# Performance work log

Measured on AMD Instinct MI355X. Metric: run time of the kernel, lower is better.

Reference implementation:

```python
import jax, jax.numpy as jnp
import numpy as np

DROPOUT_P = 0.1
DROPOUT_KEY = jax.random.key(42)


def setup_inputs() -> dict:
    key = jax.random.key(0)
    kq, kk, kv = jax.random.split(key, 3)
    B, S, H, D = 2, 2048, 16, 64
    query = jax.random.normal(kq, (B, S, H, D), dtype=jnp.float32)
    k_in = jax.random.normal(kk, (B, S, H, D), dtype=jnp.float32)
    value = jax.random.normal(kv, (B, S, H, D), dtype=jnp.float32)
    inv_scale_factor = jnp.asarray(8.0, dtype=jnp.float32)  # sqrt(head_dim)
    return {"query": query, "key": k_in, "value": value,
            "inv_scale_factor": inv_scale_factor}


def reference(query, key, value, inv_scale_factor):
    # permute(0,2,1,3): [B, S, H, D] -> [B, H, S, D]
    q = jnp.transpose(query, (0, 2, 1, 3))
    k = jnp.transpose(key, (0, 2, 1, 3))
    v = jnp.transpose(value, (0, 2, 1, 3))
    # scores: [B, H, S, S]
    scores = jnp.einsum("bhsd,bhtd->bhst", q, k) / inv_scale_factor
    attn = jax.nn.softmax(scores, axis=-1)
    # dropout (train mode, inverted scaling) with a fixed key
    keep = jax.random.bernoulli(DROPOUT_KEY, 1.0 - DROPOUT_P, attn.shape)
    attn = jnp.where(keep, attn / (1.0 - DROPOUT_P), 0.0)
    # output: [B, H, S, D]
    return jnp.einsum("bhst,bhtd->bhsd", attn, v)
```

## Files before the change

kernel.cpp:

```cpp
#include <hip/hip_runtime.h>
#include <hip/hip_bf16.h>
#include <stdint.h>

typedef __attribute__((ext_vector_type(8))) short short8;
typedef __attribute__((ext_vector_type(4))) float f32x4;
typedef __attribute__((ext_vector_type(4))) uint32_t u32x4;
typedef __attribute__((ext_vector_type(2))) uint32_t u32x2;

#define KEEP_TH 0xE6666600u

__device__ __forceinline__ uint32_t pkbf(float lo, float hi) {
  uint32_t r;
  asm("v_cvt_pk_bf16_f32 %0, %1, %2" : "=v"(r) : "v"(lo), "v"(hi));
  return r;
}

__device__ __forceinline__ uint32_t tf_bits(uint32_t x1pre) {
  uint32_t x1 = x1pre;
  uint32_t x0 = x1;
  x1 = __builtin_rotateleft32(x1, 13) ^ x0;
#define R(r) { x0 += x1; x1 = __builtin_rotateleft32(x1, (r)) ^ x0; }
  R(15) R(26) R(6)
  x0 += 42u;          x1 += 0x1BD11BF0u + 1u;
  R(17) R(29) R(16) R(24)
  x0 += 0x1BD11BF0u;  x1 += 2u;
  R(13) R(15) R(26) R(6)
                      x1 += 42u + 3u;
  R(17) R(29) R(16) R(24)
  x0 += 42u;          x1 += 0x1BD11BF0u + 4u;
  R(13) R(15) R(26) R(6)
  x0 += 0x1BD11BF0u;  x1 += 5u;
#undef R
  return x0 ^ x1;
}


__global__ __launch_bounds__(256, 4)
void attn_dropout_kernel(const float* __restrict__ Qg, const float* __restrict__ Kg,
                         const float* __restrict__ Vg, const float* __restrict__ invs,
                         float* __restrict__ Out) {
  __shared__ __align__(16) uint32_t KbF[512 * 4];
  __shared__ __align__(16) uint32_t VtF[512 * 4];
  __shared__ __align__(16) uint32_t PlF[512 * 4];

  const int tid = threadIdx.x;
  const int w = tid >> 6;
  const int l = tid & 63;
  const int e = l & 15;
  const int g = l >> 4;

  const int n  = blockIdx.x;
  const int bh = (n & 7) * 4 + ((n >> 3) & 3);
  const int b  = bh >> 4;
  const int h  = bh & 15;
  const int qc = n >> 5;
  const int qbase = qc * 64;

  const float c = 1.4426950408889634f / invs[0];
  const int sq = qbase + w * 16 + e;

  short8 qf[2];
#pragma unroll
  for (int kc = 0; kc < 2; ++kc) {
    const float* qp = Qg + (((b * 2048 + sq) * 16 + h) * 64 + kc * 32 + 8 * g);
    f32x4 q0 = *(const f32x4*)qp;
    f32x4 q1 = *(const f32x4*)(qp + 4);
    u32x4 u;
    u.x = pkbf(q0.x * c, q0.y * c);
    u.y = pkbf(q0.z * c, q0.w * c);
    u.z = pkbf(q1.x * c, q1.y * c);
    u.w = pkbf(q1.z * c, q1.w * c);
    qf[kc] = __builtin_bit_cast(short8, u);
  }

  f32x4 acc[4];
#pragma unroll
  for (int dt = 0; dt < 4; ++dt) acc[dt] = (f32x4){0.f, 0.f, 0.f, 0.f};
  float ls[4] = {0.f, 0.f, 0.f, 0.f};

  const uint32_t fb = ((uint32_t)b << 26) | ((uint32_t)h << 22) | ((uint32_t)sq << 11);

  const int s_e = tid & 15, s_g = (tid >> 4) & 3, s_kc = (tid >> 6) & 1, s_T = tid >> 7;
  const int v_e = tid & 15, v_gk = (tid >> 4) & 7, v_dt = tid >> 7;

  const float* kbase = Kg + (((b * 2048 + s_T * 16 + s_e) * 16 + h) * 64 + s_kc * 32 + 8 * s_g);
  const float* vbase = Vg + (((b * 2048 + 8 * v_gk) * 16 + h) * 64 + v_dt * 16 + v_e);

  f32x4 kA[2], kB[2];
  float vR[2][8];

#pragma unroll
  for (int r2 = 0; r2 < 2; ++r2) {
    const float* p = kbase + r2 * (32 * 16 * 64);
    kA[r2] = *(const f32x4*)p;
    kB[r2] = *(const f32x4*)(p + 4);
    const float* pv = vbase + r2 * (2 * 16 * 64);
#pragma unroll
    for (int r = 0; r < 8; ++r) vR[r2][r] = pv[r * 1024 - r2 * (2 * 16 * 64) + r2 * 32];
  }

  for (int tile = 0; tile < 32; ++tile) {
    const int t0 = tile * 64;
    __syncthreads();

#pragma unroll
    for (int r2 = 0; r2 < 2; ++r2) {
      int Tk = s_T + 2 * r2;
      u32x4 u;
      u.x = pkbf(kA[r2].x, kA[r2].y);
      u.y = pkbf(kA[r2].z, kA[r2].w);
      u.z = pkbf(kB[r2].x, kB[r2].y);
      u.w = pkbf(kB[r2].z, kB[r2].w);
      *(u32x4*)&KbF[(((Tk * 2 + s_kc) * 4 + s_g) * 16 + s_e) * 4] = u;

      int dt = v_dt + 2 * r2;
      u32x4 uv;
      uv.x = pkbf(vR[r2][0], vR[r2][1]);
      uv.y = pkbf(vR[r2][2], vR[r2][3]);
      uv.z = pkbf(vR[r2][4], vR[r2][5]);
      uv.w = pkbf(vR[r2][6], vR[r2][7]);
      *(u32x4*)&VtF[((dt * 8 + v_gk) * 16 + v_e) * 4] = uv;
    }
    __syncthreads();

    if (tile + 1 < 32) {
      const int t1 = (tile + 1) * 64;
#pragma unroll
      for (int r2 = 0; r2 < 2; ++r2) {
        const float* p = kbase + (t1 + r2 * 32) * (16 * 64);
        kA[r2] = *(const f32x4*)p;
        kB[r2] = *(const f32x4*)(p + 4);
        const float* pv = vbase + (t1) * (16 * 64) + r2 * 32;
#pragma unroll
        for (int r = 0; r < 8; ++r) vR[r2][r] = pv[r * 1024];
      }
    }

#pragma unroll
    for (int Tk = 0; Tk < 4; ++Tk) {
      u32x4 ku0 = *(const u32x4*)&KbF[(((Tk * 2 + 0) * 4 + g) * 16 + e) * 4];
      u32x4 ku1 = *(const u32x4*)&KbF[(((Tk * 2 + 1) * 4 + g) * 16 + e) * 4];
      f32x4 sacc = (f32x4){0.f, 0.f, 0.f, 0.f};
      sacc = __builtin_amdgcn_mfma_f32_16x16x32_bf16(__builtin_bit_cast(short8, ku0), qf[0], sacc, 0, 0, 0);
      sacc = __builtin_amdgcn_mfma_f32_16x16x32_bf16(__builtin_bit_cast(short8, ku1), qf[1], sacc, 0, 0, 0);
      const uint32_t jT = fb + (uint32_t)(t0 + 16 * Tk + 4 * g + 42);
      float pm[4];
#pragma unroll
      for (int r = 0; r < 4; ++r) {
        uint32_t bits = tf_bits(jT + (uint32_t)r);
        float pv = __builtin_amdgcn_exp2f(sacc[r]);
        ls[r] += pv;
        pm[r] = (bits < KEEP_TH) ? pv : 0.f;
      }
      int gp = 2 * Tk + (g >> 1);
      u32x2 pw;
      pw.x = pkbf(pm[0], pm[1]);
      pw.y = pkbf(pm[2], pm[3]);
      *(u32x2*)&PlF[((w * 8 + gp) * 16 + e) * 4 + 2 * (g & 1)] = pw;
    }
    asm volatile("" ::: "memory");

#pragma unroll
    for (int kk = 0; kk < 2; ++kk) {
      u32x4 pu = *(const u32x4*)&PlF[((w * 8 + g + 4 * kk) * 16 + e) * 4];
      short8 pf = __builtin_bit_cast(short8, pu);
#pragma unroll
      for (int dt = 0; dt < 4; ++dt) {
        u32x4 vu = *(const u32x4*)&VtF[((dt * 8 + g + 4 * kk) * 16 + e) * 4];
        acc[dt] = __builtin_amdgcn_mfma_f32_16x16x32_bf16(pf, __builtin_bit_cast(short8, vu), acc[dt], 0, 0, 0);
      }
    }
  }

  float L = (ls[0] + ls[1]) + (ls[2] + ls[3]);
  L += __shfl_xor(L, 16);
  L += __shfl_xor(L, 32);
  float rinv = 1.0f / (0.9f * L);
  float rr[4];
#pragma unroll
  for (int r = 0; r < 4; ++r) rr[r] = __shfl(rinv, 4 * g + r);
#pragma unroll
  for (int dt = 0; dt < 4; ++dt)
#pragma unroll
    for (int r = 0; r < 4; ++r) {
      int s = qbase + w * 16 + 4 * g + r;
      Out[(((b * 16 + h) * 2048 + s) * 64) + dt * 16 + e] = acc[dt][r] * rr[r];
    }
}

extern "C" void kernel_launch(void* const* d_in, const int* in_sizes, int n_in,
                              void* d_out, int out_size, void* d_ws, size_t ws_size,
                              hipStream_t stream) {
  const float* q  = (const float*)d_in[0];
  const float* k  = (const float*)d_in[1];
  const float* v  = (const float*)d_in[2];
  const float* sc = (const float*)d_in[3];
  float* out = (float*)d_out;
  (void)d_ws; (void)ws_size; (void)in_sizes; (void)n_in; (void)out_size;
  attn_dropout_kernel<<<dim3(1024), dim3(256), 0, stream>>>(q, k, v, sc, out);
}
```

Baseline: 280.8 us.

## Split key range across two blocks and combine partial sums in a second kernel

When enough workspace is available, each query tile's key loop is split into two halves handled by separate blocks, doubling the grid from 1024 to 2048 blocks. Unnormalized accumulators and row sums go to workspace, and a small combine kernel adds the halves and applies the normalization. This targets under-occupancy on a device with many CUs, and the launch bound is raised from 4 to 6. The cost is an extra kernel launch plus roughly 32 MB of workspace writes and reads.

```diff
diff --git a/kernel.cpp b/kernel.cpp
--- a/kernel.cpp
+++ b/kernel.cpp
@@ -8,6 +8,11 @@
 typedef __attribute__((ext_vector_type(2))) uint32_t u32x2;
 
 #define KEEP_TH 0xE6666600u
+
+#define WS_ACC_PART 4194304
+#define WS_L_BASE   8388608
+#define WS_L_PART   65536
+#define WS_NEED_BYTES 34078720ull
 
 __device__ __forceinline__ uint32_t pkbf(float lo, float hi) {
   uint32_t r;
@@ -35,10 +40,10 @@
 }
 
 
-__global__ __launch_bounds__(256, 4)
-void attn_dropout_kernel(const float* __restrict__ Qg, const float* __restrict__ Kg,
-                         const float* __restrict__ Vg, const float* __restrict__ invs,
-                         float* __restrict__ Out) {
+__global__ __launch_bounds__(256, 6)
+void attn_main(const float* __restrict__ Qg, const float* __restrict__ Kg,
+               const float* __restrict__ Vg, const float* __restrict__ invs,
+               float* __restrict__ Out, float* __restrict__ Ws, int split) {
   __shared__ __align__(16) uint32_t KbF[512 * 4];
   __shared__ __align__(16) uint32_t VtF[512 * 4];
   __shared__ __align__(16) uint32_t PlF[512 * 4];
@@ -50,11 +55,15 @@
   const int g = l >> 4;
 
   const int n  = blockIdx.x;
-  const int bh = (n & 7) * 4 + ((n >> 3) & 3);
+  const int m  = n & 1023;
+  const int half = split ? (n >> 10) : 0;
+  const int bh = (m & 7) * 4 + ((m >> 3) & 3);
   const int b  = bh >> 4;
   const int h  = bh & 15;
-  const int qc = n >> 5;
+  const int qc = m >> 5;
   const int qbase = qc * 64;
+  const int tile_lo  = half * 16;
+  const int tile_cnt = split ? 16 : 32;
 
   const float c = 1.4426950408889634f / invs[0];
   const int sq = qbase + w * 16 + e;
@@ -89,17 +98,22 @@
   f32x4 kA[2], kB[2];
   float vR[2][8];
 
-#pragma unroll
-  for (int r2 = 0; r2 < 2; ++r2) {
-    const float* p = kbase + r2 * (32 * 16 * 64);
-    kA[r2] = *(const f32x4*)p;
-    kB[r2] = *(const f32x4*)(p + 4);
-    const float* pv = vbase + r2 * (2 * 16 * 64);
-#pragma unroll
-    for (int r = 0; r < 8; ++r) vR[r2][r] = pv[r * 1024 - r2 * (2 * 16 * 64) + r2 * 32];
-  }
-
-  for (int tile = 0; tile < 32; ++tile) {
+  auto prefetch = [&](int tile) {
+    const int tt = tile * 64;
+#pragma unroll
+    for (int r2 = 0; r2 < 2; ++r2) {
+      const float* p = kbase + (tt + r2 * 32) * 1024;
+      kA[r2] = *(const f32x4*)p;
+      kB[r2] = *(const f32x4*)(p + 4);
+      const float* pv = vbase + tt * 1024 + r2 * 32;
+#pragma unroll
+      for (int r = 0; r < 8; ++r) vR[r2][r] = pv[r * 1024];
+    }
+  };
+
+  prefetch(tile_lo);
+
+  for (int tile = tile_lo; tile < tile_lo + tile_cnt; ++tile) {
     const int t0 = tile * 64;
     __syncthreads();
 
@@ -123,18 +137,7 @@
     }
     __syncthreads();
 
-    if (tile + 1 < 32) {
-      const int t1 = (tile + 1) * 64;
-#pragma unroll
-      for (int r2 = 0; r2 < 2; ++r2) {
-        const float* p = kbase + (t1 + r2 * 32) * (16 * 64);
-        kA[r2] = *(const f32x4*)p;
-        kB[r2] = *(const f32x4*)(p + 4);
-        const float* pv = vbase + (t1) * (16 * 64) + r2 * 32;
-#pragma unroll
-        for (int r = 0; r < 8; ++r) vR[r2][r] = pv[r * 1024];
-      }
-    }
+    if (tile + 1 < tile_lo + tile_cnt) prefetch(tile + 1);
 
 #pragma unroll
     for (int Tk = 0; Tk < 4; ++Tk) {
@@ -175,17 +178,47 @@
   float L = (ls[0] + ls[1]) + (ls[2] + ls[3]);
   L += __shfl_xor(L, 16);
   L += __shfl_xor(L, 32);
+
+  if (split) {
+    const int pbase = (half * 32 + b * 16 + h) * 2048;
+#pragma unroll
+    for (int dt = 0; dt < 4; ++dt)
+#pragma unroll
+      for (int r = 0; r < 4; ++r) {
+        int s = qbase + w * 16 + 4 * g + r;
+        Ws[(pbase + s) * 64 + dt * 16 + e] = acc[dt][r];
+      }
+    if (l < 16) Ws[WS_L_BASE + half * WS_L_PART + (b * 16 + h) * 2048 + qbase + w * 16 + l] = L;
+  } else {
+    float rinv = 1.0f / (0.9f * L);
+    float rr[4];
+#pragma unroll
+    for (int r = 0; r < 4; ++r) rr[r] = __shfl(rinv, 4 * g + r);
+#pragma unroll
+    for (int dt = 0; dt < 4; ++dt)
+#pragma unroll
+      for (int r = 0; r < 4; ++r) {
+        int s = qbase + w * 16 + 4 * g + r;
+        Out[(((b * 16 + h) * 2048 + s) * 64) + dt * 16 + e] = acc[dt][r] * rr[r];
+      }
+  }
+}
+
+__global__ __launch_bounds__(256)
+void attn_combine(const float* __restrict__ Ws, float* __restrict__ Out) {
+  const int i4 = blockIdx.x * 256 + threadIdx.x;
+  const int elem = i4 * 4;
+  const int row = elem >> 6;
+  f32x4 a0 = *(const f32x4*)&Ws[elem];
+  f32x4 a1 = *(const f32x4*)&Ws[WS_ACC_PART + elem];
+  float L = Ws[WS_L_BASE + row] + Ws[WS_L_BASE + WS_L_PART + row];
   float rinv = 1.0f / (0.9f * L);
-  float rr[4];
-#pragma unroll
-  for (int r = 0; r < 4; ++r) rr[r] = __shfl(rinv, 4 * g + r);
-#pragma unroll
-  for (int dt = 0; dt < 4; ++dt)
-#pragma unroll
-    for (int r = 0; r < 4; ++r) {
-      int s = qbase + w * 16 + 4 * g + r;
-      Out[(((b * 16 + h) * 2048 + s) * 64) + dt * 16 + e] = acc[dt][r] * rr[r];
-    }
+  f32x4 o;
+  o.x = (a0.x + a1.x) * rinv;
+  o.y = (a0.y + a1.y) * rinv;
+  o.z = (a0.z + a1.z) * rinv;
+  o.w = (a0.w + a1.w) * rinv;
+  *(f32x4*)&Out[elem] = o;
 }
 
 extern "C" void kernel_launch(void* const* d_in, const int* in_sizes, int n_in,
@@ -196,6 +229,13 @@
   const float* v  = (const float*)d_in[2];
   const float* sc = (const float*)d_in[3];
   float* out = (float*)d_out;
-  (void)d_ws; (void)ws_size; (void)in_sizes; (void)n_in; (void)out_size;
-  attn_dropout_kernel<<<dim3(1024), dim3(256), 0, stream>>>(q, k, v, sc, out);
-}
+  float* ws  = (float*)d_ws;
+  (void)in_sizes; (void)n_in; (void)out_size;
+
+  if (ws_size >= WS_NEED_BYTES) {
+    attn_main<<<dim3(2048), dim3(256), 0, stream>>>(q, k, v, sc, out, ws, 1);
+    attn_combine<<<dim3(4096), dim3(256), 0, stream>>>(ws, out);
+  } else {
+    attn_main<<<dim3(1024), dim3(256), 0, stream>>>(q, k, v, sc, out, ws, 0);
+  }
+}
```

Result: slower. 304.3 us (+8.3%).
